# Optimization experiments

Measured on AMD Instinct MI355X. Metric: run time of the kernel, lower is better.

## Reference

```python
import jax, jax.numpy as jnp
import numpy as np

N = 50000          # nodes
E = 800000         # edges
D_IN = 64          # env INPUT_DIM
D_H = 64           # env HIDDEN_DIM
D_OUT = 32         # env OUTPUT_DIM
A_H = 16           # action HIDDEN_DIM
NUM_ENV = 3        # env NUM_LAYERS
TAU = 1.0          # gumbel temperature (fixed, LEARN_TEMPERATURE=False)
LN_EPS = 1e-5


def setup_inputs() -> dict:
    key = jax.random.key(0)
    ks = jax.random.split(key, 24)

    def lin(k, fan_in, fan_out):
        s = 1.0 / np.sqrt(fan_in)
        kw, kb = jax.random.split(k)
        W = jax.random.uniform(kw, (fan_in, fan_out), jnp.float32, -s, s)
        b = jax.random.uniform(kb, (fan_out,), jnp.float32, -s, s)
        return W, b

    inp = {}
    inp['x'] = jax.random.normal(ks[0], (N, D_IN), jnp.float32)
    inp['edge_index'] = jax.random.randint(ks[1], (2, E), 0, N, dtype=jnp.int32)

    inp['W_enc'], inp['b_enc'] = lin(ks[2], D_IN, D_H)
    env_W, env_b = [], []
    for l in range(NUM_ENV):
        W, b = lin(ks[3 + l], 2 * D_H, D_H)
        env_W.append(W); env_b.append(b)
    inp['env_W'] = jnp.stack(env_W)   # [NUM_ENV, 2*D_H, D_H]
    inp['env_b'] = jnp.stack(env_b)   # [NUM_ENV, D_H]
    inp['W_dec'], inp['b_dec'] = lin(ks[6], D_H, D_OUT)
    inp['ln_g'] = jnp.ones((D_H,), jnp.float32)
    inp['ln_b'] = jnp.zeros((D_H,), jnp.float32)
    inp['in_W1'], inp['in_b1'] = lin(ks[7], 2 * D_H, A_H)
    inp['in_W2'], inp['in_b2'] = lin(ks[8], 2 * A_H, 2)
    inp['out_W1'], inp['out_b1'] = lin(ks[9], 2 * D_H, A_H)
    inp['out_W2'], inp['out_b2'] = lin(ks[10], 2 * A_H, 2)
    return inp


def _layernorm(x, g, b):
    mu = jnp.mean(x, axis=-1, keepdims=True)
    var = jnp.var(x, axis=-1, keepdims=True)
    return (x - mu) * jax.lax.rsqrt(var + LN_EPS) * g + b


def _conv(x, src, dst, W, b, edge_weight=None):
    # WeightedGNNConv: gather x[src] -> (optional * edge_weight) -> scatter-add at dst -> lin(concat(x, agg))
    msg = x[src]                                   # [E, d]
    if edge_weight is not None:
        msg = msg * edge_weight[:, None]
    agg = jax.ops.segment_sum(msg, dst, num_segments=N)
    return jnp.concatenate([x, agg], axis=-1) @ W + b


def _action_net(x, src, dst, W1, b1, W2, b2):
    h = jax.nn.relu(_conv(x, src, dst, W1, b1))
    return _conv(h, src, dst, W2, b2)              # [N, 2] logits


def _gumbel_hard(logits, key, tau):
    u = jax.random.uniform(key, logits.shape, logits.dtype, 1e-20, 1.0)
    g = -jnp.log(-jnp.log(u))
    y = jax.nn.softmax((logits + g) / tau, axis=-1)
    y_hard = jax.nn.one_hot(jnp.argmax(y, axis=-1), logits.shape[-1], dtype=y.dtype)
    return y + jax.lax.stop_gradient(y_hard - y)   # straight-through


def reference(x, edge_index, W_enc, b_enc, env_W, env_b, W_dec, b_dec, ln_g, ln_b,
              in_W1, in_b1, in_W2, in_b2, out_W1, out_b1, out_W2, out_b2):
    src, dst = edge_index[0], edge_index[1]        # u, v
    h = x @ W_enc + b_enc                          # encoder (dropout is identity in eval)
    noise_key = jax.random.key(1234)
    ews = []
    for l in range(NUM_ENV):
        h = _layernorm(h, ln_g, ln_b)
        in_logits = _action_net(h, src, dst, in_W1, in_b1, in_W2, in_b2)
        out_logits = _action_net(h, src, dst, out_W1, out_b1, out_W2, out_b2)
        in_p = _gumbel_hard(in_logits, jax.random.fold_in(noise_key, 2 * l), TAU)
        out_p = _gumbel_hard(out_logits, jax.random.fold_in(noise_key, 2 * l + 1), TAU)
        # create_edge_weight: keep_in_prob[v] * keep_out_prob[u]
        ew = in_p[:, 0][dst] * out_p[:, 0][src]    # [E], values in {0,1}
        ews.append(ew)
        h = _conv(h, src, dst, env_W[l], env_b[l], edge_weight=ew)
    out = h @ W_dec + b_dec
    return out, jnp.stack(ews)
```

## Files before the change

kernel.cpp:

```cpp
#include <hip/hip_runtime.h>
#include <math.h>

static constexpr int NN = 50000;
static constexpr int EE = 800000;

typedef unsigned long long ull;

struct TF2 { unsigned a, b; };

__host__ __device__ __forceinline__ TF2 tf2x32(unsigned k0, unsigned k1,
                                               unsigned x0, unsigned x1) {
  unsigned k2 = k0 ^ k1 ^ 0x1BD11BDAu;
  x0 += k0; x1 += k1;
#define TFR(r) { x0 += x1; x1 = (x1 << (r)) | (x1 >> (32 - (r))); x1 ^= x0; }
  TFR(13) TFR(15) TFR(26) TFR(6)
  x0 += k1; x1 += k2 + 1u;
  TFR(17) TFR(29) TFR(16) TFR(24)
  x0 += k2; x1 += k0 + 2u;
  TFR(13) TFR(15) TFR(26) TFR(6)
  x0 += k0; x1 += k1 + 3u;
  TFR(17) TFR(29) TFR(16) TFR(24)
  x0 += k1; x1 += k2 + 4u;
  TFR(13) TFR(15) TFR(26) TFR(6)
  x0 += k2; x1 += k0 + 5u;
#undef TFR
  TF2 r; r.a = x0; r.b = x1; return r;
}

__device__ __forceinline__ float u01_bits(unsigned w) {
  float fl = __uint_as_float((w >> 9) | 0x3f800000u) - 1.0f;
  return fmaxf(1e-20f, fl + 1e-20f);
}

__device__ __forceinline__ float keep01(float l0, float l1, unsigned k0, unsigned k1, int node) {
  unsigned f0 = 2u * (unsigned)node, f1 = f0 + 1u;
  TF2 t0 = tf2x32(k0, k1, 0u, f0);
  TF2 t1 = tf2x32(k0, k1, 0u, f1);
  float g0 = -logf(-logf(u01_bits(t0.a ^ t0.b)));
  float g1 = -logf(-logf(u01_bits(t1.a ^ t1.b)));
  float z0 = l0 + g0, z1 = l1 + g1;
  float m  = fmaxf(z0, z1);
  float e0 = expf(z0 - m), e1 = expf(z1 - m);
  float s  = e0 + e1;
  float y0 = e0 / s, y1 = e1 / s;
  return (y1 > y0) ? 0.0f : 1.0f;
}

__global__ void k_count(const int* __restrict__ dst, int* __restrict__ deg, int e) {
  int i = blockIdx.x * blockDim.x + threadIdx.x;
  if (i < e) atomicAdd(&deg[dst[i]], 1);
}

__global__ void k_bsum(const int* __restrict__ deg, int* __restrict__ bsum, int n) {
  int i = blockIdx.x * 256 + threadIdx.x;
  int v = (i < n) ? deg[i] : 0;
  #pragma unroll
  for (int off = 32; off; off >>= 1) v += __shfl_xor(v, off, 64);
  __shared__ int ws[4];
  if ((threadIdx.x & 63) == 0) ws[threadIdx.x >> 6] = v;
  __syncthreads();
  if (threadIdx.x == 0) bsum[blockIdx.x] = ws[0] + ws[1] + ws[2] + ws[3];
}

__global__ void k_bscan(const int* __restrict__ bsum, int* __restrict__ bpref,
                        int nb, int* __restrict__ row_ptr, int n) {
  __shared__ int s[256];
  int t = threadIdx.x;
  int v = (t < nb) ? bsum[t] : 0;
  s[t] = v; __syncthreads();
  for (int off = 1; off < 256; off <<= 1) {
    int u = (t >= off) ? s[t - off] : 0;
    __syncthreads();
    s[t] += u;
    __syncthreads();
  }
  bpref[t] = s[t] - v;
  if (t == 0) row_ptr[n] = s[255];
}

__global__ void k_prefix(const int* __restrict__ deg, const int* __restrict__ bpref,
                         int* __restrict__ row_ptr, int* __restrict__ cursor, int n) {
  __shared__ int s[256];
  int t = threadIdx.x;
  int i = blockIdx.x * 256 + t;
  int v = (i < n) ? deg[i] : 0;
  s[t] = v; __syncthreads();
  for (int off = 1; off < 256; off <<= 1) {
    int u = (t >= off) ? s[t - off] : 0;
    __syncthreads();
    s[t] += u;
    __syncthreads();
  }
  if (i < n) {
    int ex = s[t] - v + bpref[blockIdx.x];
    row_ptr[i] = ex; cursor[i] = ex;
  }
}

__global__ void k_fill(const int* __restrict__ src, const int* __restrict__ dst,
                       int* __restrict__ cursor, ull* __restrict__ ce, int e) {
  int i = blockIdx.x * blockDim.x + threadIdx.x;
  if (i < e) {
    int pos = atomicAdd(&cursor[dst[i]], 1);
    ce[pos] = ((ull)(unsigned)src[i] << 20) | (unsigned)i;
  }
}

__global__ void k_enc_ln(const float* __restrict__ x, const float* __restrict__ W,
                         const float* __restrict__ bias, const float* __restrict__ g,
                         const float* __restrict__ bb, float* __restrict__ hln) {
  __shared__ float Ws[64 * 64];
  for (int i = threadIdx.x; i < 64 * 64; i += 256) Ws[i] = W[i];
  __syncthreads();
  int node = blockIdx.x * 4 + (threadIdx.x >> 6);
  int j = threadIdx.x & 63;
  const float* xr = x + (size_t)node * 64;
  float s = bias[j];
  #pragma unroll
  for (int i = 0; i < 64; i++) s = fmaf(xr[i], Ws[i * 64 + j], s);
  float t = s;
  #pragma unroll
  for (int off = 32; off; off >>= 1) t += __shfl_xor(t, off, 64);
  float mu = t * (1.0f / 64.0f);
  float d = s - mu;
  float q = d * d;
  #pragma unroll
  for (int off = 32; off; off >>= 1) q += __shfl_xor(q, off, 64);
  float rs = 1.0f / sqrtf(q * (1.0f / 64.0f) + 1e-5f);
  hln[(size_t)node * 64 + j] = d * rs * g[j] + bb[j];
}

__global__ void k_aggA(const float* __restrict__ hln, const int* __restrict__ row_ptr,
                       const ull* __restrict__ ce,
                       const float* __restrict__ inW1, const float* __restrict__ inb1,
                       const float* __restrict__ outW1, const float* __restrict__ outb1,
                       float* __restrict__ r) {
  __shared__ float Ws[128 * 32];
  __shared__ __align__(16) float st[4][128];
  int t = threadIdx.x;
  for (int i = t; i < 128 * 16; i += 256) {
    int row = i >> 4, c = i & 15;
    Ws[row * 32 + c]      = inW1[i];
    Ws[row * 32 + 16 + c] = outW1[i];
  }
  int w = t >> 6, lane = t & 63;
  int node = blockIdx.x * 4 + w;
  float hv = hln[(size_t)node * 64 + lane];
  int b = row_ptr[node], e = row_ptr[node + 1];
  float s0 = 0.f, s1 = 0.f, s2 = 0.f, s3 = 0.f;
  for (int base = b; base < e; base += 64) {
    int idx = base + lane;
    int u_l = (idx < e) ? (int)(ce[idx] >> 20) : 0;
    int cnt = min(64, e - base);
    int k = 0;
    for (; k + 4 <= cnt; k += 4) {
      int u0 = __shfl(u_l, k, 64),     u1 = __shfl(u_l, k + 1, 64),
          u2 = __shfl(u_l, k + 2, 64), u3 = __shfl(u_l, k + 3, 64);
      s0 += hln[(size_t)u0 * 64 + lane];
      s1 += hln[(size_t)u1 * 64 + lane];
      s2 += hln[(size_t)u2 * 64 + lane];
      s3 += hln[(size_t)u3 * 64 + lane];
    }
    for (; k < cnt; k++)
      s0 += hln[(size_t)__shfl(u_l, k, 64) * 64 + lane];
  }
  st[w][lane]      = hv;
  st[w][64 + lane] = (s0 + s1) + (s2 + s3);
  __syncthreads();
  int jo = lane & 31, half = lane >> 5;
  const float* sv = &st[w][half * 64];
  float acc = 0.f;
  #pragma unroll
  for (int i = 0; i < 64; i += 4) {
    float4 c4 = *(const float4*)(sv + i);
    acc = fmaf(c4.x, Ws[(half * 64 + i    ) * 32 + jo], acc);
    acc = fmaf(c4.y, Ws[(half * 64 + i + 1) * 32 + jo], acc);
    acc = fmaf(c4.z, Ws[(half * 64 + i + 2) * 32 + jo], acc);
    acc = fmaf(c4.w, Ws[(half * 64 + i + 3) * 32 + jo], acc);
  }
  acc += __shfl_xor(acc, 32, 64);
  if (half == 0) {
    float bias = (jo < 16) ? inb1[jo] : outb1[jo - 16];
    r[(size_t)node * 32 + jo] = fmaxf(acc + bias, 0.f);
  }
}

__global__ void k_aggB(const float* __restrict__ r, const int* __restrict__ row_ptr,
                       const ull* __restrict__ ce,
                       const float* __restrict__ inW2, const float* __restrict__ inb2,
                       const float* __restrict__ outW2, const float* __restrict__ outb2,
                       float* __restrict__ keep_in, float* __restrict__ keep_out,
                       unsigned ki0, unsigned ki1, unsigned ko0, unsigned ko1) {
  int t = threadIdx.x;
  int node = blockIdx.x * 8 + (t >> 5);
  int j = t & 31;
  int b = row_ptr[node], e = row_ptr[node + 1];
  float s0 = 0.f, s1 = 0.f;
  for (int base = b; base < e; base += 32) {
    int idx = base + j;
    int u_l = (idx < e) ? (int)(ce[idx] >> 20) : 0;
    int cnt = min(32, e - base);
    int k = 0;
    for (; k + 2 <= cnt; k += 2) {
      int u0 = __shfl(u_l, k, 32), u1 = __shfl(u_l, k + 1, 32);
      s0 += r[(size_t)u0 * 32 + j];
      s1 += r[(size_t)u1 * 32 + j];
    }
    if (k < cnt) s0 += r[(size_t)__shfl(u_l, k, 32) * 32 + j];
  }
  float agg = s0 + s1;
  float self = r[(size_t)node * 32 + j];
  float p0, p1;
  if (j < 16) {
    p0 = self * inW2[j * 2 + 0] + agg * inW2[(16 + j) * 2 + 0];
    p1 = self * inW2[j * 2 + 1] + agg * inW2[(16 + j) * 2 + 1];
  } else {
    int j2 = j - 16;
    p0 = self * outW2[j2 * 2 + 0] + agg * outW2[(16 + j2) * 2 + 0];
    p1 = self * outW2[j2 * 2 + 1] + agg * outW2[(16 + j2) * 2 + 1];
  }
  #pragma unroll
  for (int off = 8; off; off >>= 1) {
    p0 += __shfl_xor(p0, off, 64);
    p1 += __shfl_xor(p1, off, 64);
  }
  if (j == 0)  keep_in[node]  = keep01(p0 + inb2[0],  p1 + inb2[1],  ki0, ki1, node);
  if (j == 16) keep_out[node] = keep01(p0 + outb2[0], p1 + outb2[1], ko0, ko1, node);
}

template <bool LN>
__global__ void k_aggC(const float* __restrict__ hln, const int* __restrict__ row_ptr,
                       const ull* __restrict__ ce, const float* __restrict__ keep_in,
                       const float* __restrict__ keep_out, float* __restrict__ ew,
                       const float* __restrict__ W, const float* __restrict__ bias,
                       const float* __restrict__ g, const float* __restrict__ bb,
                       float* __restrict__ hout) {
  __shared__ __align__(16) float st[4][128];
  int t = threadIdx.x;
  int w = t >> 6, lane = t & 63;
  int node = blockIdx.x * 4 + w;
  float ki = keep_in[node];
  float hv = hln[(size_t)node * 64 + lane];
  int b = row_ptr[node], e = row_ptr[node + 1];
  float s0 = 0.f, s1 = 0.f, s2 = 0.f, s3 = 0.f;
  for (int base = b; base < e; base += 64) {
    int idx = base + lane;
    int u_l = 0; float ko_l = 0.f;
    if (idx < e) {
      ull c = ce[idx];
      u_l = (int)(c >> 20);
      ko_l = keep_out[u_l];
      ew[(unsigned)(c & 0xFFFFFu)] = ki * ko_l;
    }
    if (ki != 0.f) {
      int cnt = min(64, e - base);
      int k = 0;
      for (; k + 4 <= cnt; k += 4) {
        int u0 = __shfl(u_l, k, 64),     u1 = __shfl(u_l, k + 1, 64),
            u2 = __shfl(u_l, k + 2, 64), u3 = __shfl(u_l, k + 3, 64);
        float w0 = __shfl(ko_l, k, 64),     w1 = __shfl(ko_l, k + 1, 64),
              w2 = __shfl(ko_l, k + 2, 64), w3 = __shfl(ko_l, k + 3, 64);
        if (w0 != 0.f) s0 += hln[(size_t)u0 * 64 + lane];
        if (w1 != 0.f) s1 += hln[(size_t)u1 * 64 + lane];
        if (w2 != 0.f) s2 += hln[(size_t)u2 * 64 + lane];
        if (w3 != 0.f) s3 += hln[(size_t)u3 * 64 + lane];
      }
      for (; k < cnt; k++) {
        int u0 = __shfl(u_l, k, 64);
        float w0 = __shfl(ko_l, k, 64);
        if (w0 != 0.f) s0 += hln[(size_t)u0 * 64 + lane];
      }
    }
  }
  float s = ((s0 + s1) + (s2 + s3)) * ki;
  st[w][lane]      = hv;
  st[w][64 + lane] = s;
  float a0 = bias[lane], a1 = 0.f, a2 = 0.f, a3 = 0.f;
  #pragma unroll 4
  for (int i = 0; i < 128; i += 4) {
    float4 c4 = *(const float4*)(&st[w][i]);
    a0 = fmaf(c4.x, W[(i    ) * 64 + lane], a0);
    a1 = fmaf(c4.y, W[(i + 1) * 64 + lane], a1);
    a2 = fmaf(c4.z, W[(i + 2) * 64 + lane], a2);
    a3 = fmaf(c4.w, W[(i + 3) * 64 + lane], a3);
  }
  float acc = (a0 + a1) + (a2 + a3);
  if (LN) {
    float tt = acc;
    #pragma unroll
    for (int off = 32; off; off >>= 1) tt += __shfl_xor(tt, off, 64);
    float mu = tt * (1.0f / 64.0f);
    float d = acc - mu;
    float q = d * d;
    #pragma unroll
    for (int off = 32; off; off >>= 1) q += __shfl_xor(q, off, 64);
    float rs = 1.0f / sqrtf(q * (1.0f / 64.0f) + 1e-5f);
    hout[(size_t)node * 64 + lane] = d * rs * g[lane] + bb[lane];
  } else {
    hout[(size_t)node * 64 + lane] = acc;
  }
}

__global__ void k_dec(const float* __restrict__ h, const float* __restrict__ W,
                      const float* __restrict__ bias, float* __restrict__ out) {
  __shared__ float Ws[64 * 32];
  int t = threadIdx.x;
  for (int i = t; i < 64 * 32; i += 256) Ws[i] = W[i];
  __syncthreads();
  int node = blockIdx.x * 8 + (t >> 5);
  int j = t & 31;
  const float* hr = h + (size_t)node * 64;
  float s = bias[j];
  #pragma unroll
  for (int i = 0; i < 64; i++) s = fmaf(hr[i], Ws[i * 32 + j], s);
  out[(size_t)node * 32 + j] = s;
}

extern "C" void kernel_launch(void* const* d_in, const int* in_sizes, int n_in,
                              void* d_out, int out_size, void* d_ws, size_t ws_size,
                              hipStream_t stream) {
  const float* x      = (const float*)d_in[0];
  const int*   ei     = (const int*)  d_in[1];
  const float* W_enc  = (const float*)d_in[2];
  const float* b_enc  = (const float*)d_in[3];
  const float* env_W  = (const float*)d_in[4];
  const float* env_b  = (const float*)d_in[5];
  const float* W_dec  = (const float*)d_in[6];
  const float* b_dec  = (const float*)d_in[7];
  const float* ln_g   = (const float*)d_in[8];
  const float* ln_b   = (const float*)d_in[9];
  const float* in_W1  = (const float*)d_in[10];
  const float* in_b1  = (const float*)d_in[11];
  const float* in_W2  = (const float*)d_in[12];
  const float* in_b2  = (const float*)d_in[13];
  const float* out_W1 = (const float*)d_in[14];
  const float* out_b1 = (const float*)d_in[15];
  const float* out_W2 = (const float*)d_in[16];
  const float* out_b2 = (const float*)d_in[17];

  const int n = NN, e = EE;
  const int* src = ei;
  const int* dst = ei + e;

  float* out_h  = (float*)d_out;
  float* out_ew = out_h + (size_t)n * 32;

  size_t off = 0;
  auto alloc = [&](size_t bytes) -> void* {
    void* p = (char*)d_ws + off;
    off += (bytes + 255) & ~(size_t)255;
    return p;
  };
  float* hlnA    = (float*)alloc((size_t)n * 64 * 4);
  float* hlnB    = (float*)alloc((size_t)n * 64 * 4);
  float* r       = (float*)alloc((size_t)n * 32 * 4);
  float* keep_i  = (float*)alloc((size_t)n * 4);
  float* keep_o  = (float*)alloc((size_t)n * 4);
  int*   deg     = (int*)alloc((size_t)n * 4);
  int*   row_ptr = (int*)alloc((size_t)(n + 1) * 4);
  int*   cursor  = (int*)alloc((size_t)n * 4);
  int*   bsum    = (int*)alloc(256 * 4);
  int*   bpref   = (int*)alloc(256 * 4);
  ull*   ce      = (ull*)alloc((size_t)e * 8);
  if (off > ws_size) return;

  const int nb = (n + 255) / 256;

  hipMemsetAsync(deg, 0, (size_t)n * 4, stream);
  k_count<<<(e + 255) / 256, 256, 0, stream>>>(dst, deg, e);
  k_bsum<<<nb, 256, 0, stream>>>(deg, bsum, n);
  k_bscan<<<1, 256, 0, stream>>>(bsum, bpref, nb, row_ptr, n);
  k_prefix<<<nb, 256, 0, stream>>>(deg, bpref, row_ptr, cursor, n);
  k_fill<<<(e + 255) / 256, 256, 0, stream>>>(src, dst, cursor, ce, e);

  const int g4 = n / 4;
  const int g8 = n / 8;

  k_enc_ln<<<g4, 256, 0, stream>>>(x, W_enc, b_enc, ln_g, ln_b, hlnA);

  float* hln = hlnA;
  float* hln_next = hlnB;
  for (int l = 0; l < 3; l++) {
    TF2 kin  = tf2x32(0u, 1234u, 0u, (unsigned)(2 * l));
    TF2 kout = tf2x32(0u, 1234u, 0u, (unsigned)(2 * l + 1));

    k_aggA<<<g4, 256, 0, stream>>>(hln, row_ptr, ce, in_W1, in_b1, out_W1, out_b1, r);
    k_aggB<<<g8, 256, 0, stream>>>(r, row_ptr, ce, in_W2, in_b2, out_W2, out_b2,
                                   keep_i, keep_o, kin.a, kin.b, kout.a, kout.b);
    if (l < 2) {
      k_aggC<true><<<g4, 256, 0, stream>>>(hln, row_ptr, ce, keep_i, keep_o,
                                           out_ew + (size_t)l * e,
                                           env_W + (size_t)l * 128 * 64,
                                           env_b + (size_t)l * 64, ln_g, ln_b, hln_next);
    } else {
      k_aggC<false><<<g4, 256, 0, stream>>>(hln, row_ptr, ce, keep_i, keep_o,
                                            out_ew + (size_t)l * e,
                                            env_W + (size_t)l * 128 * 64,
                                            env_b + (size_t)l * 64, ln_g, ln_b, hln_next);
    }
    float* tmp = hln; hln = hln_next; hln_next = tmp;
  }

  k_dec<<<g8, 256, 0, stream>>>(hln, W_dec, b_dec, out_h);
}
```

Baseline: 704.4 us.

## Project features before aggregation in action nets to shrink gather width

The action-network convolutions now apply the linear layer before aggregation, using linearity: h is first projected to 32-wide self and neighbour parts, so the first gather reads 32 floats per edge instead of 64. The second layer is also projected first, to 8 floats per node, so its gather reads a float4 per edge. This cuts gather bandwidth but adds one extra kernel and extra intermediate buffers, and changes the floating-point summation order. Separately, the env conv kernel now stages its 128x64 weight matrix in shared memory instead of reading it from global memory.

After: 708.2 us. No clear change (+0.5%).

```diff
diff --git a/kernel.cpp b/kernel.cpp
--- a/kernel.cpp
+++ b/kernel.cpp
@@ -130,70 +130,40 @@
   hln[(size_t)node * 64 + j] = d * rs * g[j] + bb[j];
 }
 
-__global__ void k_aggA(const float* __restrict__ hln, const int* __restrict__ row_ptr,
-                       const ull* __restrict__ ce,
-                       const float* __restrict__ inW1, const float* __restrict__ inb1,
-                       const float* __restrict__ outW1, const float* __restrict__ outb1,
-                       float* __restrict__ r) {
-  __shared__ float Ws[128 * 32];
-  __shared__ __align__(16) float st[4][128];
-  int t = threadIdx.x;
-  for (int i = t; i < 128 * 16; i += 256) {
-    int row = i >> 4, c = i & 15;
-    Ws[row * 32 + c]      = inW1[i];
-    Ws[row * 32 + 16 + c] = outW1[i];
-  }
+__global__ void k_proj(const float* __restrict__ hln,
+                       const float* __restrict__ W1i, const float* __restrict__ W1o,
+                       float* __restrict__ P1, float* __restrict__ S1, int nchunk) {
+  int t = threadIdx.x, w = t >> 6, lane = t & 63;
+  int h = lane >> 5, jo = lane & 31;
+  const float* Wg = (jo < 16) ? W1i : W1o;
+  int col = jo & 15;
+  float wr[64];
+  #pragma unroll
+  for (int i = 0; i < 64; i++) wr[i] = Wg[(h * 64 + i) * 16 + col];
+  __shared__ float st[256];
+  for (int blk = blockIdx.x; blk < nchunk; blk += gridDim.x) {
+    __syncthreads();
+    st[t] = hln[(size_t)blk * 256 + t];
+    __syncthreads();
+    const float* sv = &st[w * 64];
+    float a = 0.f;
+    #pragma unroll
+    for (int i = 0; i < 64; i++) a = fmaf(sv[i], wr[i], a);
+    size_t node = (size_t)blk * 4 + w;
+    if (h == 0) S1[node * 32 + jo] = a;
+    else        P1[node * 32 + jo] = a;
+  }
+}
+
+__global__ void k_gatherA(const float* __restrict__ P1, const float* __restrict__ S1,
+                          const int* __restrict__ row_ptr, const ull* __restrict__ ce,
+                          const float* __restrict__ inb1, const float* __restrict__ outb1,
+                          const float* __restrict__ inW2, const float* __restrict__ outW2,
+                          float* __restrict__ P2S2) {
+  int t = threadIdx.x;
   int w = t >> 6, lane = t & 63;
-  int node = blockIdx.x * 4 + w;
-  float hv = hln[(size_t)node * 64 + lane];
-  int b = row_ptr[node], e = row_ptr[node + 1];
-  float s0 = 0.f, s1 = 0.f, s2 = 0.f, s3 = 0.f;
-  for (int base = b; base < e; base += 64) {
-    int idx = base + lane;
-    int u_l = (idx < e) ? (int)(ce[idx] >> 20) : 0;
-    int cnt = min(64, e - base);
-    int k = 0;
-    for (; k + 4 <= cnt; k += 4) {
-      int u0 = __shfl(u_l, k, 64),     u1 = __shfl(u_l, k + 1, 64),
-          u2 = __shfl(u_l, k + 2, 64), u3 = __shfl(u_l, k + 3, 64);
-      s0 += hln[(size_t)u0 * 64 + lane];
-      s1 += hln[(size_t)u1 * 64 + lane];
-      s2 += hln[(size_t)u2 * 64 + lane];
-      s3 += hln[(size_t)u3 * 64 + lane];
-    }
-    for (; k < cnt; k++)
-      s0 += hln[(size_t)__shfl(u_l, k, 64) * 64 + lane];
-  }
-  st[w][lane]      = hv;
-  st[w][64 + lane] = (s0 + s1) + (s2 + s3);
-  __syncthreads();
-  int jo = lane & 31, half = lane >> 5;
-  const float* sv = &st[w][half * 64];
-  float acc = 0.f;
-  #pragma unroll
-  for (int i = 0; i < 64; i += 4) {
-    float4 c4 = *(const float4*)(sv + i);
-    acc = fmaf(c4.x, Ws[(half * 64 + i    ) * 32 + jo], acc);
-    acc = fmaf(c4.y, Ws[(half * 64 + i + 1) * 32 + jo], acc);
-    acc = fmaf(c4.z, Ws[(half * 64 + i + 2) * 32 + jo], acc);
-    acc = fmaf(c4.w, Ws[(half * 64 + i + 3) * 32 + jo], acc);
-  }
-  acc += __shfl_xor(acc, 32, 64);
-  if (half == 0) {
-    float bias = (jo < 16) ? inb1[jo] : outb1[jo - 16];
-    r[(size_t)node * 32 + jo] = fmaxf(acc + bias, 0.f);
-  }
-}
-
-__global__ void k_aggB(const float* __restrict__ r, const int* __restrict__ row_ptr,
-                       const ull* __restrict__ ce,
-                       const float* __restrict__ inW2, const float* __restrict__ inb2,
-                       const float* __restrict__ outW2, const float* __restrict__ outb2,
-                       float* __restrict__ keep_in, float* __restrict__ keep_out,
-                       unsigned ki0, unsigned ki1, unsigned ko0, unsigned ko1) {
-  int t = threadIdx.x;
-  int node = blockIdx.x * 8 + (t >> 5);
-  int j = t & 31;
+  int sub = lane >> 5, j = lane & 31;
+  int node = blockIdx.x * 8 + w * 2 + sub;
   int b = row_ptr[node], e = row_ptr[node + 1];
   float s0 = 0.f, s1 = 0.f;
   for (int base = b; base < e; base += 32) {
@@ -203,29 +173,67 @@
     int k = 0;
     for (; k + 2 <= cnt; k += 2) {
       int u0 = __shfl(u_l, k, 32), u1 = __shfl(u_l, k + 1, 32);
-      s0 += r[(size_t)u0 * 32 + j];
-      s1 += r[(size_t)u1 * 32 + j];
+      s0 += P1[(size_t)u0 * 32 + j];
+      s1 += P1[(size_t)u1 * 32 + j];
     }
-    if (k < cnt) s0 += r[(size_t)__shfl(u_l, k, 32) * 32 + j];
+    if (k < cnt) s0 += P1[(size_t)__shfl(u_l, k, 32) * 32 + j];
   }
   float agg = s0 + s1;
-  float self = r[(size_t)node * 32 + j];
-  float p0, p1;
+  float b1j = (j < 16) ? inb1[j] : outb1[j - 16];
+  float rj = fmaxf(S1[(size_t)node * 32 + j] + agg + b1j, 0.f);
+  float wa0, wa1, wb0, wb1;
   if (j < 16) {
-    p0 = self * inW2[j * 2 + 0] + agg * inW2[(16 + j) * 2 + 0];
-    p1 = self * inW2[j * 2 + 1] + agg * inW2[(16 + j) * 2 + 1];
+    wa0 = inW2[j * 2 + 0];  wa1 = inW2[j * 2 + 1];
+    wb0 = inW2[(16 + j) * 2 + 0];  wb1 = inW2[(16 + j) * 2 + 1];
   } else {
     int j2 = j - 16;
-    p0 = self * outW2[j2 * 2 + 0] + agg * outW2[(16 + j2) * 2 + 0];
-    p1 = self * outW2[j2 * 2 + 1] + agg * outW2[(16 + j2) * 2 + 1];
-  }
+    wa0 = outW2[j2 * 2 + 0];  wa1 = outW2[j2 * 2 + 1];
+    wb0 = outW2[(16 + j2) * 2 + 0];  wb1 = outW2[(16 + j2) * 2 + 1];
+  }
+  float v0 = rj * wa0, v1 = rj * wa1, v2 = rj * wb0, v3 = rj * wb1;
   #pragma unroll
   for (int off = 8; off; off >>= 1) {
-    p0 += __shfl_xor(p0, off, 64);
-    p1 += __shfl_xor(p1, off, 64);
-  }
-  if (j == 0)  keep_in[node]  = keep01(p0 + inb2[0],  p1 + inb2[1],  ki0, ki1, node);
-  if (j == 16) keep_out[node] = keep01(p0 + outb2[0], p1 + outb2[1], ko0, ko1, node);
+    v0 += __shfl_xor(v0, off, 64);
+    v1 += __shfl_xor(v1, off, 64);
+    v2 += __shfl_xor(v2, off, 64);
+    v3 += __shfl_xor(v3, off, 64);
+  }
+  float* row = P2S2 + (size_t)node * 8;
+  if (j == 0)  { row[0] = v2; row[1] = v3; row[4] = v0; row[5] = v1; }
+  if (j == 16) { row[2] = v2; row[3] = v3; row[6] = v0; row[7] = v1; }
+}
+
+__global__ void k_gatherB(const float* __restrict__ P2S2, const int* __restrict__ row_ptr,
+                          const ull* __restrict__ ce,
+                          const float* __restrict__ inb2, const float* __restrict__ outb2,
+                          float* __restrict__ keep_in, float* __restrict__ keep_out,
+                          unsigned ki0, unsigned ki1, unsigned ko0, unsigned ko1) {
+  int t = threadIdx.x;
+  int w = t >> 6, lane = t & 63;
+  int g = lane >> 4, el = lane & 15;
+  int node = blockIdx.x * 16 + w * 4 + g;
+  int b = row_ptr[node], e = row_ptr[node + 1];
+  float a0 = 0.f, a1 = 0.f, a2 = 0.f, a3 = 0.f;
+  for (int base = b; base < e; base += 16) {
+    int idx = base + el;
+    if (idx < e) {
+      int u = (int)(ce[idx] >> 20);
+      float4 p = *(const float4*)(P2S2 + (size_t)u * 8);
+      a0 += p.x; a1 += p.y; a2 += p.z; a3 += p.w;
+    }
+  }
+  #pragma unroll
+  for (int off = 8; off; off >>= 1) {
+    a0 += __shfl_xor(a0, off, 64);
+    a1 += __shfl_xor(a1, off, 64);
+    a2 += __shfl_xor(a2, off, 64);
+    a3 += __shfl_xor(a3, off, 64);
+  }
+  float4 sf = *(const float4*)(P2S2 + (size_t)node * 8 + 4);
+  if (el == 0)
+    keep_in[node]  = keep01(sf.x + a0 + inb2[0],  sf.y + a1 + inb2[1],  ki0, ki1, node);
+  else if (el == 1)
+    keep_out[node] = keep01(sf.z + a2 + outb2[0], sf.w + a3 + outb2[1], ko0, ko1, node);
 }
 
 template <bool LN>
@@ -235,8 +243,11 @@
                        const float* __restrict__ W, const float* __restrict__ bias,
                        const float* __restrict__ g, const float* __restrict__ bb,
                        float* __restrict__ hout) {
+  __shared__ float Ws[128 * 64];
   __shared__ __align__(16) float st[4][128];
   int t = threadIdx.x;
+  for (int i = t; i < 128 * 64; i += 256) Ws[i] = W[i];
+  __syncthreads();
   int w = t >> 6, lane = t & 63;
   int node = blockIdx.x * 4 + w;
   float ki = keep_in[node];
@@ -279,10 +290,10 @@
   #pragma unroll 4
   for (int i = 0; i < 128; i += 4) {
     float4 c4 = *(const float4*)(&st[w][i]);
-    a0 = fmaf(c4.x, W[(i    ) * 64 + lane], a0);
-    a1 = fmaf(c4.y, W[(i + 1) * 64 + lane], a1);
-    a2 = fmaf(c4.z, W[(i + 2) * 64 + lane], a2);
-    a3 = fmaf(c4.w, W[(i + 3) * 64 + lane], a3);
+    a0 = fmaf(c4.x, Ws[(i    ) * 64 + lane], a0);
+    a1 = fmaf(c4.y, Ws[(i + 1) * 64 + lane], a1);
+    a2 = fmaf(c4.z, Ws[(i + 2) * 64 + lane], a2);
+    a3 = fmaf(c4.w, Ws[(i + 3) * 64 + lane], a3);
   }
   float acc = (a0 + a1) + (a2 + a3);
   if (LN) {
@@ -353,7 +364,9 @@
   };
   float* hlnA    = (float*)alloc((size_t)n * 64 * 4);
   float* hlnB    = (float*)alloc((size_t)n * 64 * 4);
-  float* r       = (float*)alloc((size_t)n * 32 * 4);
+  float* P1      = (float*)alloc((size_t)n * 32 * 4);
+  float* S1      = (float*)alloc((size_t)n * 32 * 4);
+  float* P2S2    = (float*)alloc((size_t)n * 8 * 4);
   float* keep_i  = (float*)alloc((size_t)n * 4);
   float* keep_o  = (float*)alloc((size_t)n * 4);
   int*   deg     = (int*)alloc((size_t)n * 4);
@@ -373,8 +386,9 @@
   k_prefix<<<nb, 256, 0, stream>>>(deg, bpref, row_ptr, cursor, n);
   k_fill<<<(e + 255) / 256, 256, 0, stream>>>(src, dst, cursor, ce, e);
 
-  const int g4 = n / 4;
-  const int g8 = n / 8;
+  const int g4  = n / 4;
+  const int g8  = n / 8;
+  const int g16 = n / 16;
 
   k_enc_ln<<<g4, 256, 0, stream>>>(x, W_enc, b_enc, ln_g, ln_b, hlnA);
 
@@ -384,9 +398,11 @@
     TF2 kin  = tf2x32(0u, 1234u, 0u, (unsigned)(2 * l));
     TF2 kout = tf2x32(0u, 1234u, 0u, (unsigned)(2 * l + 1));
 
-    k_aggA<<<g4, 256, 0, stream>>>(hln, row_ptr, ce, in_W1, in_b1, out_W1, out_b1, r);
-    k_aggB<<<g8, 256, 0, stream>>>(r, row_ptr, ce, in_W2, in_b2, out_W2, out_b2,
-                                   keep_i, keep_o, kin.a, kin.b, kout.a, kout.b);
+    k_proj<<<1250, 256, 0, stream>>>(hln, in_W1, out_W1, P1, S1, g4);
+    k_gatherA<<<g8, 256, 0, stream>>>(P1, S1, row_ptr, ce, in_b1, out_b1,
+                                      in_W2, out_W2, P2S2);
+    k_gatherB<<<g16, 256, 0, stream>>>(P2S2, row_ptr, ce, in_b2, out_b2,
+                                       keep_i, keep_o, kin.a, kin.b, kout.a, kout.b);
     if (l < 2) {
       k_aggC<true><<<g4, 256, 0, stream>>>(hln, row_ptr, ce, keep_i, keep_o,
                                            out_ew + (size_t)l * e,
```
